# Kernel optimization log

Hardware: AMD Instinct MI355X
Metric: run time of the kernel (lower is better)

Reference implementation:

```python
import jax, jax.numpy as jnp
import numpy as np

N_NODES = 100000
N_EDGES = 3200000
IN_DIM = 128
HIDDEN = 64
NUM_COLORS = 10


def setup_inputs() -> dict:
    key = jax.random.key(0)
    ks = jax.random.split(key, 10)
    x = jax.random.normal(ks[0], (N_NODES, IN_DIM), dtype=jnp.float32)
    edge_index = jax.random.randint(ks[1], (2, N_EDGES), 0, N_NODES, dtype=jnp.int64)
    action_mask = jax.random.randint(ks[2], (N_NODES, NUM_COLORS), 0, 2) > 0
    # GCNConv weights (glorot-ish scale) and biases
    W1 = jax.random.normal(ks[3], (IN_DIM, HIDDEN), dtype=jnp.float32) / np.sqrt(IN_DIM)
    b1 = jnp.zeros((HIDDEN,), dtype=jnp.float32)
    W2 = jax.random.normal(ks[4], (HIDDEN, HIDDEN), dtype=jnp.float32) / np.sqrt(HIDDEN)
    b2 = jnp.zeros((HIDDEN,), dtype=jnp.float32)
    Wh = jax.random.normal(ks[5], (HIDDEN, NUM_COLORS), dtype=jnp.float32) / np.sqrt(HIDDEN)
    bh = jnp.zeros((NUM_COLORS,), dtype=jnp.float32)
    return {"x": x, "edge_index": edge_index, "action_mask": action_mask,
            "W1": W1, "b1": b1, "W2": W2, "b2": b2, "Wh": Wh, "bh": bh}


def _gcn_conv(x, src, dst, dinv, W, b, n_nodes):
    """PyG GCNConv: out = D^-1/2 (A+I) D^-1/2 (x W) + b, self-loops already in src/dst."""
    h = x @ W                                   # [N, H]
    norm = dinv[src] * dinv[dst]                # [E+N]
    msg = h[src] * norm[:, None]                # gather + scale
    out = jax.ops.segment_sum(msg, dst, num_segments=n_nodes)  # scatter-add at targets
    return out + b


def reference(x, edge_index, action_mask, W1, b1, W2, b2, Wh, bh):
    n = x.shape[0]
    loops = jnp.arange(n, dtype=edge_index.dtype)
    src = jnp.concatenate([edge_index[0], loops])   # sources (with self-loops)
    dst = jnp.concatenate([edge_index[1], loops])   # targets
    deg = jax.ops.segment_sum(jnp.ones(dst.shape, x.dtype), dst, num_segments=n)
    dinv = deg ** -0.5                              # deg >= 1 thanks to self-loops

    h = jax.nn.relu(_gcn_conv(x, src, dst, dinv, W1, b1, n))
    h = jax.nn.relu(_gcn_conv(h, src, dst, dinv, W2, b2, n))
    logits = h @ Wh + bh                            # [N, num_colors]

    logits_flat = logits.reshape(-1)
    mask_flat = action_mask.reshape(-1)
    return jnp.where(mask_flat, logits_flat, jnp.finfo(logits_flat.dtype).min)
```

## Files before the change

kernel.cpp:

```cpp
#include <hip/hip_runtime.h>
#include <float.h>
#include <math.h>


#define MASKED_VAL (-3.3895313892515355e+38f)
#define SHIFT 7
#define BNODES 128
#define CHUNK 8192
#define DCAP 6144
#define NBP 800

typedef unsigned short u16;

static __device__ __forceinline__ float bf2f(u16 u) {
  union { unsigned int i; float f; } x;
  x.i = ((unsigned int)u) << 16;
  return x.f;
}
static __device__ __forceinline__ u16 f2bf(float f) {
  union { float f; unsigned int i; } x;
  x.f = f;
  unsigned int i = x.i;
  return (u16)((i + 0x7FFFu + ((i >> 16) & 1u)) >> 16);
}

__global__ __launch_bounds__(256) void chunk_hist(const int* __restrict__ dst,
                                                  int* __restrict__ hist,
                                                  int E, int Nn, int NB) {
  __shared__ int h[NBP];
  int t = threadIdx.x;
  int c0 = blockIdx.x * CHUNK;
  int end = c0 + CHUNK < E ? c0 + CHUNK : E;
  for (int i = t; i < NB; i += 256) h[i] = 0;
  __syncthreads();
  for (int i = c0 + t; i < end; i += 256) {
    int d = dst[i];
    if ((unsigned)d >= (unsigned)Nn) d = 0;
    atomicAdd(&h[d >> SHIFT], 1);
  }
  __syncthreads();
  size_t row = (size_t)blockIdx.x * NBP;
  for (int i = t; i < NB; i += 256) hist[row + i] = h[i];
}

__global__ __launch_bounds__(256) void col_scan(const int* __restrict__ hist,
                                                int* __restrict__ cbbase,
                                                int* __restrict__ bcnt, int nch,
                                                const unsigned char* __restrict__ m,
                                                int* __restrict__ mflag, int NB) {
  __shared__ int sm[256];
  __shared__ int nzoff;
  int b = blockIdx.x;
  int t = threadIdx.x;
  if (b == NB) {
    if (t == 0) nzoff = 0;
    __syncthreads();
    for (int i = t; i < 4096; i += 256)
      if ((i & 3) && m[i]) atomicAdd(&nzoff, 1);
    __syncthreads();
    if (t == 0) *mflag = (nzoff == 0) ? 1 : 0;
    return;
  }
  int carry = 0;
  for (int tile = 0; tile < nch; tile += 256) {
    int c = tile + t;
    int v = (c < nch) ? hist[(size_t)c * NBP + b] : 0;
    sm[t] = v;
    __syncthreads();
    for (int off = 1; off < 256; off <<= 1) {
      int add = (t >= off) ? sm[t - off] : 0;
      __syncthreads();
      sm[t] += add;
      __syncthreads();
    }
    if (c < nch) cbbase[(size_t)c * NBP + b] = carry + sm[t] - v;
    carry += sm[255];
    __syncthreads();
  }
  if (t == 0) bcnt[b] = carry;
}

__global__ __launch_bounds__(256) void chunk_sort_scatter(const int* __restrict__ src,
                                                          const int* __restrict__ dst,
                                                          const int* __restrict__ hist,
                                                          const int* __restrict__ cbbase,
                                                          int* __restrict__ pairs,
                                                          int E, int Nn, int NB) {
  __shared__ int h[NBP];
  __shared__ int base[NBP + 1];
  __shared__ int cur[NBP];
  __shared__ int dp[NBP];
  __shared__ int ts[256];
  __shared__ int sorted[CHUNK];
  int t = threadIdx.x;
  int c0 = blockIdx.x * CHUNK;
  int end = c0 + CHUNK < E ? c0 + CHUNK : E;
  int n = end - c0;
  size_t row = (size_t)blockIdx.x * NBP;
  for (int i = t; i < NB; i += 256) h[i] = hist[row + i];
  __syncthreads();
  int v0 = 0, v1 = 0, v2 = 0, v3 = 0, s = 0;
  {
    int b4 = t * 4;
    if (b4 + 0 < NB) { v0 = h[b4 + 0]; s += v0; }
    if (b4 + 1 < NB) { v1 = h[b4 + 1]; s += v1; }
    if (b4 + 2 < NB) { v2 = h[b4 + 2]; s += v2; }
    if (b4 + 3 < NB) { v3 = h[b4 + 3]; s += v3; }
  }
  ts[t] = s;
  __syncthreads();
  for (int off = 1; off < 256; off <<= 1) {
    int add = (t >= off) ? ts[t - off] : 0;
    __syncthreads();
    ts[t] += add;
    __syncthreads();
  }
  {
    int run = t ? ts[t - 1] : 0;
    int b4 = t * 4;
    if (b4 + 0 < NB) { base[b4 + 0] = run; cur[b4 + 0] = run; run += v0; }
    if (b4 + 1 < NB) { base[b4 + 1] = run; cur[b4 + 1] = run; run += v1; }
    if (b4 + 2 < NB) { base[b4 + 2] = run; cur[b4 + 2] = run; run += v2; }
    if (b4 + 3 < NB) { base[b4 + 3] = run; cur[b4 + 3] = run; run += v3; }
  }
  if (t == 0) base[NB] = n;
  __syncthreads();
  for (int i = t; i < NB; i += 256) dp[i] = i * DCAP + cbbase[row + i] - base[i];
  __syncthreads();
  for (int i = c0 + t; i < end; i += 256) {
    int d = dst[i];
    if ((unsigned)d >= (unsigned)Nn) d = 0;
    int sv = src[i];
    if ((unsigned)sv >= (unsigned)Nn) sv = 0;
    int b = d >> SHIFT;
    int r = atomicAdd(&cur[b], 1);
    sorted[r] = ((d & (BNODES - 1)) << 25) | sv;
  }
  __syncthreads();
  for (int i = t; i < n; i += 256) {
    int lo = 0, hi = NB;
    while (hi - lo > 1) {
      int mid = (lo + hi) >> 1;
      if (base[mid] <= i) lo = mid; else hi = mid;
    }
    int p = dp[lo] + i;
    if (p < (lo + 1) * DCAP) pairs[p] = sorted[i];
  }
}

__global__ __launch_bounds__(256) void bucket_build(const int* __restrict__ pairs,
                                                    const int* __restrict__ bcnt,
                                                    int* __restrict__ counts,
                                                    int* __restrict__ offs,
                                                    float* __restrict__ dinv,
                                                    int* __restrict__ csr, int Nn) {
  __shared__ int pl[DCAP];
  __shared__ int cl[BNODES], ol[BNODES], cu[BNODES];
  int t = threadIdx.x;
  int b = blockIdx.x;
  int cnt = bcnt[b];
  if (cnt > DCAP) cnt = DCAP;
  int base = b * DCAP;
  for (int i = t; i < cnt; i += 256) pl[i] = pairs[base + i];
  if (t < BNODES) {
    cl[t] = 0;
    cu[t] = 0;
  }
  __syncthreads();
  for (int i = t; i < cnt; i += 256) atomicAdd(&cl[(unsigned)pl[i] >> 25], 1);
  __syncthreads();
  int v = (t < BNODES) ? cl[t] : 0;
  if (t < BNODES) ol[t] = v;
  __syncthreads();
  for (int off = 1; off < BNODES; off <<= 1) {
    int add = (t >= off && t < BNODES) ? ol[t - off] : 0;
    __syncthreads();
    if (t < BNODES) ol[t] += add;
    __syncthreads();
  }
  if (t < BNODES) {
    int excl = ol[t] - v;
    ol[t] = excl;
    int node = (b << SHIFT) + t;
    if (node < Nn) {
      counts[node] = v;
      offs[node] = base + excl;
      dinv[node] = 1.0f / sqrtf((float)(v + 1));
    }
  }
  __syncthreads();
  for (int i = t; i < cnt; i += 256) {
    int p = pl[i];
    int dl = (unsigned)p >> 25;
    int r = atomicAdd(&cu[dl], 1);
    csr[base + ol[dl] + r] = p & 0x1FFFFFF;
  }
}

template <int K, bool BF_IN>
__global__ __launch_bounds__(256) void gemm_scaled(const void* __restrict__ Xv,
                                                   const float* __restrict__ W,
                                                   const float* __restrict__ dinv,
                                                   u16* __restrict__ out, int nN) {
  __shared__ float xsT[64][68];
  __shared__ float ws[64][68];
  const int t = threadIdx.x;
  const int nbase = blockIdx.x * 64;
  const int gn = t >> 4;
  const int gc = t & 15;
  float acc[4][4] = {};
  for (int kc = 0; kc < K; kc += 64) {
    __syncthreads();
#pragma unroll
    for (int it = 0; it < 4; ++it) {
      int L = it * 256 + t;
      int node = L >> 4;
      int kq = L & 15;
      int n = nbase + node;
      if (n >= nN) n = nN - 1;
      if (BF_IN) {
        const u16* X = (const u16*)Xv;
        ushort4 v = *(const ushort4*)(X + (size_t)n * K + kc + kq * 4);
        xsT[kq * 4 + 0][node] = bf2f(v.x);
        xsT[kq * 4 + 1][node] = bf2f(v.y);
        xsT[kq * 4 + 2][node] = bf2f(v.z);
        xsT[kq * 4 + 3][node] = bf2f(v.w);
      } else {
        const float* X = (const float*)Xv;
        float4 v = *(const float4*)(X + (size_t)n * K + kc + kq * 4);
        xsT[kq * 4 + 0][node] = v.x;
        xsT[kq * 4 + 1][node] = v.y;
        xsT[kq * 4 + 2][node] = v.z;
        xsT[kq * 4 + 3][node] = v.w;
      }
      int wk = L >> 4;
      int wc = (L & 15) * 4;
      float4 wv = *(const float4*)(W + (size_t)(kc + wk) * 64 + wc);
      *(float4*)&ws[wk][wc] = wv;
    }
    __syncthreads();
#pragma unroll
    for (int k = 0; k < 64; ++k) {
      float4 xa = *(const float4*)&xsT[k][gn * 4];
      float4 wa = *(const float4*)&ws[k][gc * 4];
      float xr[4] = {xa.x, xa.y, xa.z, xa.w};
      float wr[4] = {wa.x, wa.y, wa.z, wa.w};
#pragma unroll
      for (int i = 0; i < 4; ++i)
#pragma unroll
        for (int j = 0; j < 4; ++j) acc[i][j] += xr[i] * wr[j];
    }
  }
#pragma unroll
  for (int i = 0; i < 4; ++i) {
    int n = nbase + gn * 4 + i;
    if (n < nN) {
      float s = dinv[n];
      ushort4 o;
      o.x = f2bf(acc[i][0] * s);
      o.y = f2bf(acc[i][1] * s);
      o.z = f2bf(acc[i][2] * s);
      o.w = f2bf(acc[i][3] * s);
      *(ushort4*)(out + (size_t)n * 64 + gc * 4) = o;
    }
  }
}

#define GATHER_BODY(hs)                                                        \
  int wave_l = threadIdx.x >> 6;                                               \
  int lane = threadIdx.x & 63;                                                 \
  int sub = lane >> 4;                                                         \
  int l16 = lane & 15;                                                         \
  int ln = wave_l * 4 + sub;                       \
  int node = blockIdx.x * 16 + ln;                                             \
  bool alive = node < nN;                                                      \
  int nd = alive ? node : (nN - 1);                                            \
  int beg = offs[nd];                                                          \
  int c = cnt[nd];                                                             \
  ushort4 sv = *(const ushort4*)(hs + (size_t)nd * 64 + l16 * 4);              \
  float a0 = bf2f(sv.x), a1 = bf2f(sv.y), a2 = bf2f(sv.z), a3 = bf2f(sv.w);    \
  float b0 = 0.f, b1 = 0.f, b2 = 0.f, b3 = 0.f;                                \
  int j = 0;                                                                   \
  for (; j + 8 <= c; j += 8) {                                                 \
    int s0 = csr[beg + j + 0];                                                 \
    int s1 = csr[beg + j + 1];                                                 \
    int s2 = csr[beg + j + 2];                                                 \
    int s3 = csr[beg + j + 3];                                                 \
    int s4 = csr[beg + j + 4];                                                 \
    int s5 = csr[beg + j + 5];                                                 \
    int s6 = csr[beg + j + 6];                                                 \
    int s7 = csr[beg + j + 7];                                                 \
    ushort4 v0 = *(const ushort4*)(hs + (size_t)s0 * 64 + l16 * 4);            \
    ushort4 v1 = *(const ushort4*)(hs + (size_t)s1 * 64 + l16 * 4);            \
    ushort4 v2 = *(const ushort4*)(hs + (size_t)s2 * 64 + l16 * 4);            \
    ushort4 v3 = *(const ushort4*)(hs + (size_t)s3 * 64 + l16 * 4);            \
    ushort4 v4 = *(const ushort4*)(hs + (size_t)s4 * 64 + l16 * 4);            \
    ushort4 v5 = *(const ushort4*)(hs + (size_t)s5 * 64 + l16 * 4);            \
    ushort4 v6 = *(const ushort4*)(hs + (size_t)s6 * 64 + l16 * 4);            \
    ushort4 v7 = *(const ushort4*)(hs + (size_t)s7 * 64 + l16 * 4);            \
    a0 += bf2f(v0.x); a1 += bf2f(v0.y); a2 += bf2f(v0.z); a3 += bf2f(v0.w);    \
    b0 += bf2f(v1.x); b1 += bf2f(v1.y); b2 += bf2f(v1.z); b3 += bf2f(v1.w);    \
    a0 += bf2f(v2.x); a1 += bf2f(v2.y); a2 += bf2f(v2.z); a3 += bf2f(v2.w);    \
    b0 += bf2f(v3.x); b1 += bf2f(v3.y); b2 += bf2f(v3.z); b3 += bf2f(v3.w);    \
    a0 += bf2f(v4.x); a1 += bf2f(v4.y); a2 += bf2f(v4.z); a3 += bf2f(v4.w);    \
    b0 += bf2f(v5.x); b1 += bf2f(v5.y); b2 += bf2f(v5.z); b3 += bf2f(v5.w);    \
    a0 += bf2f(v6.x); a1 += bf2f(v6.y); a2 += bf2f(v6.z); a3 += bf2f(v6.w);    \
    b0 += bf2f(v7.x); b1 += bf2f(v7.y); b2 += bf2f(v7.z); b3 += bf2f(v7.w);    \
  }                                                                            \
  for (; j < c; ++j) {                                                         \
    int s = csr[beg + j];                                                      \
    ushort4 v = *(const ushort4*)(hs + (size_t)s * 64 + l16 * 4);              \
    a0 += bf2f(v.x); a1 += bf2f(v.y); a2 += bf2f(v.z); a3 += bf2f(v.w);        \
  }                                                                            \
  a0 += b0; a1 += b1; a2 += b2; a3 += b3;                                      \
  float dv = dinv[nd];                                                         \
  float4 bv = *(const float4*)(bias + l16 * 4);                                \
  float r0 = dv * a0 + bv.x;                                                   \
  float r1 = dv * a1 + bv.y;                                                   \
  float r2 = dv * a2 + bv.z;                                                   \
  float r3 = dv * a3 + bv.w;                                                   \
  r0 = r0 > 0.f ? r0 : 0.f;                                                    \
  r1 = r1 > 0.f ? r1 : 0.f;                                                    \
  r2 = r2 > 0.f ? r2 : 0.f;                                                    \
  r3 = r3 > 0.f ? r3 : 0.f;

__global__ __launch_bounds__(256) void aggregate_gemm(const u16* __restrict__ hs1,
                                                      const int* __restrict__ csr,
                                                      const int* __restrict__ offs,
                                                      const int* __restrict__ cnt,
                                                      const float* __restrict__ dinv,
                                                      const float* __restrict__ bias,
                                                      const float* __restrict__ W2,
                                                      u16* __restrict__ hs2, int nN) {
  __shared__ float w2s[64][64];
  __shared__ float h1s[16][68];
  {
    int t = threadIdx.x;
    for (int i = t; i < 1024; i += 256) {
      float4 wv = *(const float4*)(W2 + (size_t)i * 4);
      *(float4*)&w2s[i >> 4][(i & 15) * 4] = wv;
    }
  }
  __syncthreads();
  GATHER_BODY(hs1)
  int c4 = l16 * 4;
  h1s[ln][c4 + 0] = r0;
  h1s[ln][c4 + 1] = r1;
  h1s[ln][c4 + 2] = r2;
  h1s[ln][c4 + 3] = r3;
  float o0 = 0.f, o1 = 0.f, o2 = 0.f, o3 = 0.f;
#pragma unroll 4
  for (int k = 0; k < 64; ++k) {
    float hv = h1s[ln][k];
    float4 wr = *(const float4*)&w2s[k][c4];
    o0 += hv * wr.x;
    o1 += hv * wr.y;
    o2 += hv * wr.z;
    o3 += hv * wr.w;
  }
  if (alive) {
    ushort4 o;
    o.x = f2bf(o0 * dv);
    o.y = f2bf(o1 * dv);
    o.z = f2bf(o2 * dv);
    o.w = f2bf(o3 * dv);
    *(ushort4*)(hs2 + (size_t)nd * 64 + c4) = o;
  }
}

__global__ __launch_bounds__(256) void aggregate_head(const u16* __restrict__ hs2,
                                                      const int* __restrict__ csr,
                                                      const int* __restrict__ offs,
                                                      const int* __restrict__ cnt,
                                                      const float* __restrict__ dinv,
                                                      const float* __restrict__ bias,
                                                      const float* __restrict__ Wh,
                                                      const float* __restrict__ bh,
                                                      const unsigned char* __restrict__ mask,
                                                      const int* __restrict__ mflag,
                                                      float* __restrict__ out, int nN) {
  __shared__ float whs[640];
  __shared__ float bhs[16];
  __shared__ float h2s[16][68];
  {
    int t = threadIdx.x;
    for (int i = t; i < 640; i += 256) whs[i] = Wh[i];
    if (t < 10) bhs[t] = bh[t];
  }
  __syncthreads();
  GATHER_BODY(hs2)
  int c4 = l16 * 4;
  h2s[ln][c4 + 0] = r0;
  h2s[ln][c4 + 1] = r1;
  h2s[ln][c4 + 2] = r2;
  h2s[ln][c4 + 3] = r3;
  if (alive && l16 < 10) {
    float acc = bhs[l16];
#pragma unroll 4
    for (int k = 0; k < 64; ++k) acc += h2s[ln][k] * whs[k * 10 + l16];
    size_t idx = (size_t)nd * 10 + l16;
    bool mv = (*mflag) ? (((const int*)mask)[idx] != 0) : (mask[idx] != 0);
    out[idx] = mv ? acc : MASKED_VAL;
  }
}

extern "C" void kernel_launch(void* const* d_in, const int* in_sizes, int n_in,
                              void* d_out, int out_size, void* d_ws, size_t ws_size,
                              hipStream_t stream) {
  const float* x = (const float*)d_in[0];
  const int* ei = (const int*)d_in[1];
  const unsigned char* mask = (const unsigned char*)d_in[2];
  const float* W1 = (const float*)d_in[3];
  const float* b1 = (const float*)d_in[4];
  const float* W2 = (const float*)d_in[5];
  const float* b2 = (const float*)d_in[6];
  const float* Wh = (const float*)d_in[7];
  const float* bh = (const float*)d_in[8];
  float* out = (float*)d_out;

  const int N = in_sizes[0] / 128;
  const int E = in_sizes[1] / 2;
  const int* src = ei;
  const int* dst = ei + E;
  const int NB = (N + BNODES - 1) >> SHIFT;
  const int nchunks = (E + CHUNK - 1) / CHUNK;

  char* w = (char*)d_ws;
  auto alloc = [&](size_t bytes) {
    void* p = (void*)w;
    w += (bytes + 255) / 256 * 256;
    return p;
  };
  int* counts = (int*)alloc((size_t)N * 4);
  int* offs = (int*)alloc((size_t)N * 4);
  float* dinv = (float*)alloc((size_t)N * 4);
  int* bcnt = (int*)alloc(1024 * 4);
  int* mflag = (int*)alloc(4);
  int* hist = (int*)alloc((size_t)nchunks * NBP * 4);
  int* cbbase = (int*)alloc((size_t)nchunks * NBP * 4);
  int* csr = (int*)alloc((size_t)NB * DCAP * 4);
  u16* bufA = (u16*)alloc((size_t)N * 64 * 2);
  size_t pairs_bytes = (size_t)NB * DCAP * 4;
  size_t bufB_bytes = (size_t)N * 64 * 2;
  void* shared_raw = alloc(pairs_bytes > bufB_bytes ? pairs_bytes : bufB_bytes);
  u16* bufB = (u16*)shared_raw;
  int* pairs = (int*)shared_raw;

  const int ablocks = (N + 15) / 16;

  chunk_hist<<<nchunks, 256, 0, stream>>>(dst, hist, E, N, NB);
  col_scan<<<NB + 1, 256, 0, stream>>>(hist, cbbase, bcnt, nchunks, mask, mflag, NB);
  chunk_sort_scatter<<<nchunks, 256, 0, stream>>>(src, dst, hist, cbbase,
                                                  pairs, E, N, NB);
  bucket_build<<<NB, 256, 0, stream>>>(pairs, bcnt, counts, offs, dinv, csr, N);

  gemm_scaled<128, false><<<(N + 63) / 64, 256, 0, stream>>>(x, W1, dinv, bufA, N);
  aggregate_gemm<<<ablocks, 256, 0, stream>>>(bufA, csr, offs, counts, dinv, b1,
                                              W2, bufB, N);
  aggregate_head<<<ablocks, 256, 0, stream>>>(bufB, csr, offs, counts, dinv, b2,
                                              Wh, bh, mask, mflag, out, N);
}
```

Measured before the change: 240.1 us.

## Degree-sort nodes within buckets for balanced gather and store W2 as bf16

bucket_build now counting-sorts each 128-node bucket by in-degree and writes a permutation, and both aggregation kernels process nodes in that order. Lanes in a wave then handle nodes with similar degree, which cuts divergence in the neighbour-gather loop. W2 in shared memory is also stored as bf16 instead of float, halving its LDS footprint and read width. The costs are an extra indirection load per node, a less contiguous write pattern, and slightly reduced W2 precision.

```diff
diff --git a/kernel.cpp b/kernel.cpp
--- a/kernel.cpp
+++ b/kernel.cpp
@@ -153,9 +153,11 @@
                                                     int* __restrict__ counts,
                                                     int* __restrict__ offs,
                                                     float* __restrict__ dinv,
-                                                    int* __restrict__ csr, int Nn) {
+                                                    int* __restrict__ csr,
+                                                    int* __restrict__ perm, int Nn) {
   __shared__ int pl[DCAP];
   __shared__ int cl[BNODES], ol[BNODES], cu[BNODES];
+  __shared__ int dh[BNODES], dsc[BNODES], dcur[BNODES];
   int t = threadIdx.x;
   int b = blockIdx.x;
   int cnt = bcnt[b];
@@ -165,6 +167,8 @@
   if (t < BNODES) {
     cl[t] = 0;
     cu[t] = 0;
+    dh[t] = 0;
+    dcur[t] = 0;
   }
   __syncthreads();
   for (int i = t; i < cnt; i += 256) atomicAdd(&cl[(unsigned)pl[i] >> 25], 1);
@@ -178,10 +182,10 @@
     if (t < BNODES) ol[t] += add;
     __syncthreads();
   }
+  int node = (b << SHIFT) + t;
   if (t < BNODES) {
     int excl = ol[t] - v;
     ol[t] = excl;
-    int node = (b << SHIFT) + t;
     if (node < Nn) {
       counts[node] = v;
       offs[node] = base + excl;
@@ -194,6 +198,22 @@
     int dl = (unsigned)p >> 25;
     int r = atomicAdd(&cu[dl], 1);
     csr[base + ol[dl] + r] = p & 0x1FFFFFF;
+  }
+  int degb = v < 127 ? v : 127;
+  if (t < BNODES && node < Nn) atomicAdd(&dh[degb], 1);
+  __syncthreads();
+  int dv_ = (t < BNODES) ? dh[t] : 0;
+  if (t < BNODES) dsc[t] = dv_;
+  __syncthreads();
+  for (int off = 1; off < BNODES; off <<= 1) {
+    int add = (t >= off && t < BNODES) ? dsc[t - off] : 0;
+    __syncthreads();
+    if (t < BNODES) dsc[t] += add;
+    __syncthreads();
+  }
+  if (t < BNODES && node < Nn) {
+    int rank = (dsc[degb] - dh[degb]) + atomicAdd(&dcur[degb], 1);
+    perm[(b << SHIFT) + rank] = node;
   }
 }
 
@@ -272,9 +292,9 @@
   int sub = lane >> 4;                                                         \
   int l16 = lane & 15;                                                         \
   int ln = wave_l * 4 + sub;                       \
-  int node = blockIdx.x * 16 + ln;                                             \
-  bool alive = node < nN;                                                      \
-  int nd = alive ? node : (nN - 1);                                            \
+  int pidx = blockIdx.x * 16 + ln;                                             \
+  bool alive = pidx < nN;                                                      \
+  int nd = perm[alive ? pidx : (nN - 1)];                                      \
   int beg = offs[nd];                                                          \
   int c = cnt[nd];                                                             \
   ushort4 sv = *(const ushort4*)(hs + (size_t)nd * 64 + l16 * 4);              \
@@ -331,14 +351,20 @@
                                                       const float* __restrict__ dinv,
                                                       const float* __restrict__ bias,
                                                       const float* __restrict__ W2,
+                                                      const int* __restrict__ perm,
                                                       u16* __restrict__ hs2, int nN) {
-  __shared__ float w2s[64][64];
+  __shared__ u16 w2s[64][64];
   __shared__ float h1s[16][68];
   {
     int t = threadIdx.x;
     for (int i = t; i < 1024; i += 256) {
       float4 wv = *(const float4*)(W2 + (size_t)i * 4);
-      *(float4*)&w2s[i >> 4][(i & 15) * 4] = wv;
+      ushort4 o;
+      o.x = f2bf(wv.x);
+      o.y = f2bf(wv.y);
+      o.z = f2bf(wv.z);
+      o.w = f2bf(wv.w);
+      *(ushort4*)&w2s[i >> 4][(i & 15) * 4] = o;
     }
   }
   __syncthreads();
@@ -352,11 +378,11 @@
 #pragma unroll 4
   for (int k = 0; k < 64; ++k) {
     float hv = h1s[ln][k];
-    float4 wr = *(const float4*)&w2s[k][c4];
-    o0 += hv * wr.x;
-    o1 += hv * wr.y;
-    o2 += hv * wr.z;
-    o3 += hv * wr.w;
+    ushort4 wr = *(const ushort4*)&w2s[k][c4];
+    o0 += hv * bf2f(wr.x);
+    o1 += hv * bf2f(wr.y);
+    o2 += hv * bf2f(wr.z);
+    o3 += hv * bf2f(wr.w);
   }
   if (alive) {
     ushort4 o;
@@ -378,6 +404,7 @@
                                                       const float* __restrict__ bh,
                                                       const unsigned char* __restrict__ mask,
                                                       const int* __restrict__ mflag,
+                                                      const int* __restrict__ perm,
                                                       float* __restrict__ out, int nN) {
   __shared__ float whs[640];
   __shared__ float bhs[16];
@@ -434,6 +461,7 @@
   int* counts = (int*)alloc((size_t)N * 4);
   int* offs = (int*)alloc((size_t)N * 4);
   float* dinv = (float*)alloc((size_t)N * 4);
+  int* perm = (int*)alloc((size_t)N * 4);
   int* bcnt = (int*)alloc(1024 * 4);
   int* mflag = (int*)alloc(4);
   int* hist = (int*)alloc((size_t)nchunks * NBP * 4);
@@ -452,11 +480,11 @@
   col_scan<<<NB + 1, 256, 0, stream>>>(hist, cbbase, bcnt, nchunks, mask, mflag, NB);
   chunk_sort_scatter<<<nchunks, 256, 0, stream>>>(src, dst, hist, cbbase,
                                                   pairs, E, N, NB);
-  bucket_build<<<NB, 256, 0, stream>>>(pairs, bcnt, counts, offs, dinv, csr, N);
+  bucket_build<<<NB, 256, 0, stream>>>(pairs, bcnt, counts, offs, dinv, csr, perm, N);
 
   gemm_scaled<128, false><<<(N + 63) / 64, 256, 0, stream>>>(x, W1, dinv, bufA, N);
   aggregate_gemm<<<ablocks, 256, 0, stream>>>(bufA, csr, offs, counts, dinv, b1,
-                                              W2, bufB, N);
+                                              W2, perm, bufB, N);
   aggregate_head<<<ablocks, 256, 0, stream>>>(bufB, csr, offs, counts, dinv, b2,
-                                              Wh, bh, mask, mflag, out, N);
-}
+                                              Wh, bh, mask, mflag, perm, out, N);
+}
```

After: 255.9 us. 1.07x slower.
